# Kernel tuning notes

Hardware: AMD Instinct MI355X
Metric: run time of the kernel (lower is better)

## Reference

```python
import jax, jax.numpy as jnp
from jax import lax
import numpy as np

B, C, H, W = 4, 256, 64, 64
SPLIT = 8           # split_size
HEADS_BR = 4        # num_heads // 2 per branch
C2 = C // 2         # per-branch channels
HID = 4 * C         # mlp hidden
EPS = 1e-5


def layernorm(x, w, b):
    m = jnp.mean(x, -1, keepdims=True)
    v = jnp.mean((x - m) ** 2, -1, keepdims=True)
    return (x - m) * lax.rsqrt(v + EPS) * w + b


def lepe_attn(qk, v, gw, gb, Hsp, Wsp):
    # qk, v: (B, L, Cb) with L = H*W; windows of (Hsp, Wsp)
    Bq, L, Cb = qk.shape
    heads, hd = HEADS_BR, Cb // HEADS_BR
    nH, nW = H // Hsp, W // Wsp
    scale = hd ** -0.5
    # tokens -> windows -> heads: (B*nH*nW, heads, Hsp*Wsp, hd)
    qkw = (qk.reshape(Bq, nH, Hsp, nW, Wsp, Cb)
             .transpose(0, 1, 3, 2, 4, 5)
             .reshape(-1, Hsp * Wsp, heads, hd)
             .transpose(0, 2, 1, 3))
    # v as window images (B*nH*nW, Cb, Hsp, Wsp) for depthwise LePE conv
    vimg = (v.reshape(Bq, nH, Hsp, nW, Wsp, Cb)
              .transpose(0, 1, 3, 5, 2, 4)
              .reshape(-1, Cb, Hsp, Wsp))
    lepe = lax.conv_general_dilated(
        vimg, gw, (1, 1), 'SAME',
        dimension_numbers=('NCHW', 'OIHW', 'NCHW'),
        feature_group_count=Cb) + gb[None, :, None, None]
    vwin = vimg.reshape(-1, heads, hd, Hsp * Wsp).transpose(0, 1, 3, 2)
    lep = lepe.reshape(-1, heads, hd, Hsp * Wsp).transpose(0, 1, 3, 2)
    attn = jax.nn.softmax(
        jnp.einsum('whqd,whkd->whqk', qkw * scale, qkw), axis=-1)
    out = jnp.einsum('whqk,whkd->whqd', attn, vwin) + lep
    # windows -> image -> tokens
    out = (out.transpose(0, 2, 1, 3)
              .reshape(Bq, nH, nW, Hsp, Wsp, Cb)
              .transpose(0, 1, 3, 2, 4, 5)
              .reshape(Bq, L, Cb))
    return out


def setup_inputs() -> dict:
    key = jax.random.key(0)
    ks = jax.random.split(key, 8)
    p = lambda k, s: jax.random.normal(k, s, jnp.float32) * 0.02
    return {
        'x': jax.random.normal(ks[0], (B, C, H, W), jnp.float32),
        'norm1_w': jnp.ones((C,), jnp.float32),
        'norm1_b': jnp.zeros((C,), jnp.float32),
        'qkv_w': p(ks[1], (2 * C, C)),
        'getv_w0': p(ks[2], (C2, 1, 3, 3)),
        'getv_b0': jnp.zeros((C2,), jnp.float32),
        'getv_w1': p(ks[3], (C2, 1, 3, 3)),
        'getv_b1': jnp.zeros((C2,), jnp.float32),
        'proj_w': p(ks[4], (C, C)),
        'proj_b': jnp.zeros((C,), jnp.float32),
        'norm2_w': jnp.ones((C,), jnp.float32),
        'norm2_b': jnp.zeros((C,), jnp.float32),
        'fc1_w': p(ks[5], (HID, C)),
        'fc1_b': jnp.zeros((HID,), jnp.float32),
        'fc2_w': p(ks[6], (C, HID)),
        'fc2_b': jnp.zeros((C,), jnp.float32),
    }


def reference(x, norm1_w, norm1_b, qkv_w, getv_w0, getv_b0, getv_w1, getv_b1,
              proj_w, proj_b, norm2_w, norm2_b, fc1_w, fc1_b, fc2_w, fc2_b):
    b, c, h, w = x.shape
    x = x.reshape(b, c, h * w).transpose(0, 2, 1)        # (B, L, C)
    img = layernorm(x, norm1_w, norm1_b)
    qkv = img @ qkv_w.T                                  # (B, L, 2C)
    qk, v = qkv[..., :c], qkv[..., c:]                   # shared q=k, and v
    # branch 0: windows (H, split); branch 1: windows (split, W)
    x1 = lepe_attn(qk[..., :C2], v[..., :C2], getv_w0, getv_b0, h, SPLIT)
    x2 = lepe_attn(qk[..., C2:], v[..., C2:], getv_w1, getv_b1, SPLIT, w)
    att = jnp.concatenate([x1, x2], axis=2) @ proj_w.T + proj_b
    x = x + att
    y = layernorm(x, norm2_w, norm2_b)
    y = jax.nn.gelu(y @ fc1_w.T + fc1_b, approximate=False) @ fc2_w.T + fc2_b
    return x + y                                          # (B, L, C)
```

## Files before the change

kernel.cpp:

```cpp
#include <hip/hip_runtime.h>
#include <hip/hip_bf16.h>

#define BDIM 4
#define CDIM 256
#define HDIM 64
#define WDIM 64
#define LDIM 4096
#define ROWS 16384

typedef __attribute__((ext_vector_type(8))) short short8;
typedef __attribute__((ext_vector_type(4))) float f32x4;
typedef __attribute__((ext_vector_type(16))) float f32x16;
typedef unsigned int u32;

static __device__ __forceinline__ unsigned short f2bf(float f) {
    unsigned int x = __float_as_uint(f);
    unsigned int r = (x + 0x7fffu + ((x >> 16) & 1u)) >> 16;
    return (unsigned short)r;
}
static __device__ __forceinline__ float bf2f(unsigned int u) {
    return __uint_as_float(u << 16);
}
static __device__ __forceinline__ u32 pk2(float a, float b) {
    return (u32)f2bf(a) | ((u32)f2bf(b) << 16);
}

__global__ __launch_bounds__(256) void cvt4_kernel(
    const float* __restrict__ a, const float* __restrict__ b,
    const float* __restrict__ c, const float* __restrict__ d,
    unsigned short* __restrict__ oa, unsigned short* __restrict__ ob,
    unsigned short* __restrict__ oc, unsigned short* __restrict__ od)
{
    int i = blockIdx.x * 256 + threadIdx.x;
    const float* in; unsigned short* out; int off;
    if (i < 32768)       { in = a; out = oa; off = i; }
    else if (i < 49152)  { in = b; out = ob; off = i - 32768; }
    else if (i < 114688) { in = c; out = oc; off = i - 49152; }
    else if (i < 180224) { in = d; out = od; off = i - 114688; }
    else return;
    float4 f = reinterpret_cast<const float4*>(in)[off];
    reinterpret_cast<uint2*>(out)[off] = make_uint2(pk2(f.x, f.y), pk2(f.z, f.w));
}

__global__ __launch_bounds__(256) void norm_kernel(
    const float* __restrict__ xin,
    const float* __restrict__ w, const float* __restrict__ b,
    unsigned short* __restrict__ out,
    float* __restrict__ xT,
    int transposed_in)
{
    int wave = threadIdx.x >> 6;
    int lane = threadIdx.x & 63;
    int row = blockIdx.x * 4 + wave;
    float v[4];
    float sum = 0.f, sumsq = 0.f;
    if (transposed_in) {
        int bb = row >> 12;
        int l = row & 4095;
        const float* xb = xin + (size_t)bb * (CDIM * LDIM) + l;
        #pragma unroll
        for (int i = 0; i < 4; ++i) {
            int c = lane + i * 64;
            float t = xb[(size_t)c * LDIM];
            v[i] = t; sum += t; sumsq += t * t;
        }
    } else {
        const float* xr = xin + (size_t)row * CDIM;
        #pragma unroll
        for (int i = 0; i < 4; ++i) {
            float t = xr[lane + i * 64];
            v[i] = t; sum += t; sumsq += t * t;
        }
    }
    #pragma unroll
    for (int off = 32; off > 0; off >>= 1) {
        sum   += __shfl_xor(sum, off);
        sumsq += __shfl_xor(sumsq, off);
    }
    float mean = sum * (1.f / 256.f);
    float var  = sumsq * (1.f / 256.f) - mean * mean;
    float inv  = rsqrtf(var + 1e-5f);
    unsigned short* orow = out + (size_t)row * CDIM;
    #pragma unroll
    for (int i = 0; i < 4; ++i) {
        int c = lane + i * 64;
        if (xT) xT[(size_t)row * CDIM + c] = v[i];
        orow[c] = f2bf((v[i] - mean) * inv * w[c] + b[c]);
    }
}

__global__ __launch_bounds__(256) void mfma_gemm(
    const unsigned short* __restrict__ A,
    const unsigned short* __restrict__ Bm,
    const float* __restrict__ bias,
    const float* __restrict__ resid,
    void* __restrict__ outp,
    int N, int K, int mode)
{
    __shared__ unsigned short As[2][64 * 32];
    __shared__ unsigned short Bs[2][64 * 32];
    int tid  = threadIdx.x;
    int lane = tid & 63;
    int w    = tid >> 6;
    int wr   = w >> 1, wc = w & 1;
    int l15  = lane & 15, kbl = lane >> 4;

    int gx  = gridDim.x;
    int nwg = gx * gridDim.y;
    int bid = blockIdx.y * gx + blockIdx.x;
    int cpx = nwg >> 3;
    int swz = (bid & 7) * cpx + (bid >> 3);
    int n0 = (swz % gx) * 64;
    int m0 = (swz / gx) * 64;

    f32x4 acc[2][2];
    #pragma unroll
    for (int m = 0; m < 2; ++m)
        #pragma unroll
        for (int n = 0; n < 2; ++n)
            acc[m][n] = (f32x4){0.f, 0.f, 0.f, 0.f};

    int srow = tid >> 2;
    int sp   = tid & 3;
    int ss   = sp ^ (srow & 3);
    auto STAGE = [&](int buf, int k0) {
        const unsigned short* ga = A  + (size_t)(m0 + srow) * K + k0 + ss * 8;
        const unsigned short* gb = Bm + (size_t)(n0 + srow) * K + k0 + ss * 8;
        __builtin_amdgcn_global_load_lds(
            (const __attribute__((address_space(1))) void*)ga,
            (__attribute__((address_space(3))) void*)(As[buf] + tid * 8), 16, 0, 0);
        __builtin_amdgcn_global_load_lds(
            (const __attribute__((address_space(1))) void*)gb,
            (__attribute__((address_space(3))) void*)(Bs[buf] + tid * 8), 16, 0, 0);
    };

    STAGE(0, 0);
    __syncthreads();

    int cur = 0;
    for (int k0 = 0; k0 < K; k0 += 32) {
        if (k0 + 32 < K) STAGE(cur ^ 1, k0 + 32);

        short8 af[2], bf[2];
        #pragma unroll
        for (int m = 0; m < 2; ++m) {
            int row = wr * 32 + m * 16 + l15;
            af[m] = *reinterpret_cast<const short8*>(
                As[cur] + row * 32 + (kbl ^ (row & 3)) * 8);
        }
        #pragma unroll
        for (int n = 0; n < 2; ++n) {
            int row = wc * 32 + n * 16 + l15;
            bf[n] = *reinterpret_cast<const short8*>(
                Bs[cur] + row * 32 + (kbl ^ (row & 3)) * 8);
        }
        #pragma unroll
        for (int m = 0; m < 2; ++m)
            #pragma unroll
            for (int n = 0; n < 2; ++n)
                acc[m][n] = __builtin_amdgcn_mfma_f32_16x16x32_bf16(
                    af[m], bf[n], acc[m][n], 0, 0, 0);

        __syncthreads();
        cur ^= 1;
    }

    int r0 = kbl * 4;
    #pragma unroll
    for (int m = 0; m < 2; ++m) {
        #pragma unroll
        for (int n = 0; n < 2; ++n) {
            int col = n0 + wc * 32 + n * 16 + l15;
            #pragma unroll
            for (int r = 0; r < 4; ++r) {
                int row = m0 + wr * 32 + m * 16 + r0 + r;
                float v = acc[m][n][r];
                if (mode == 0) {
                    ((float*)outp)[(size_t)row * N + col] = v;
                } else if (mode == 1) {
                    ((unsigned short*)outp)[(size_t)row * N + col] = f2bf(v);
                } else if (mode == 2) {
                    v += bias[col];
                    v = 0.5f * v * (1.f + erff(v * 0.70710678118654752f));
                    ((unsigned short*)outp)[(size_t)row * N + col] = f2bf(v);
                } else {
                    v += bias[col] + resid[(size_t)row * N + col];
                    ((float*)outp)[(size_t)row * N + col] = v;
                }
            }
        }
    }
}

__global__ __launch_bounds__(512) void attn_kernel(
    const unsigned short* __restrict__ qkv,
    const float* __restrict__ gw0, const float* __restrict__ gb0,
    const float* __restrict__ gw1, const float* __restrict__ gb1,
    unsigned short* __restrict__ att)
{
    __shared__ unsigned short Kbuf[512 * 32];
    __shared__ unsigned short Vt[32 * 512];
    __shared__ float gwl[288];
    __shared__ float gbl[32];
    const int wh = blockIdx.x;
    const int br = wh >> 7, head = wh & 3, win = (wh >> 2) & 31;
    const int bb = win >> 3, wi = win & 7;
    const int tid = threadIdx.x;
    const int qk_off = br * 128 + head * 32;
    const int v_off = 256 + qk_off;
    const float sscale = 0.42044820762685725f;

    {
        const float* gw = br ? gw1 : gw0;
        const float* gb = br ? gb1 : gb0;
        if (tid < 288) gwl[tid] = gw[(head * 32) * 9 + tid];
        else if (tid >= 480) gbl[tid - 480] = gb[head * 32 + tid - 480];
    }
    {
        int t = tid;
        int l = (br == 0) ? ((t >> 3) * 64 + wi * 8 + (t & 7)) : (wi * 512 + t);
        const unsigned short* src = qkv + ((size_t)(bb * 4096 + l)) * 512 + qk_off;
        #pragma unroll
        for (int s = 0; s < 4; ++s) {
            uint4 raw = *reinterpret_cast<const uint4*>(src + s * 8);
            u32 rw[4] = {raw.x, raw.y, raw.z, raw.w};
            u32 ow[4];
            #pragma unroll
            for (int i = 0; i < 4; ++i) {
                float lo = bf2f(rw[i] & 0xffffu) * sscale;
                float hi = bf2f(rw[i] >> 16) * sscale;
                ow[i] = pk2(lo, hi);
            }
            int sl = s ^ ((t >> 1) & 3);
            *reinterpret_cast<uint4*>(Kbuf + t * 32 + sl * 8) =
                make_uint4(ow[0], ow[1], ow[2], ow[3]);
        }
    }
    {
        int kp = (tid & 255) * 2, dh = tid >> 8;
        int kq = kp + 1;
        int l0 = (br == 0) ? ((kp >> 3) * 64 + wi * 8 + (kp & 7)) : (wi * 512 + kp);
        int l1 = (br == 0) ? ((kq >> 3) * 64 + wi * 8 + (kq & 7)) : (wi * 512 + kq);
        const unsigned short* v0 = qkv + ((size_t)(bb * 4096 + l0)) * 512 + v_off + dh * 16;
        const unsigned short* v1 = qkv + ((size_t)(bb * 4096 + l1)) * 512 + v_off + dh * 16;
        uint4 a0 = *reinterpret_cast<const uint4*>(v0);
        uint4 a1 = *reinterpret_cast<const uint4*>(v0 + 8);
        uint4 b0 = *reinterpret_cast<const uint4*>(v1);
        uint4 b1 = *reinterpret_cast<const uint4*>(v1 + 8);
        u32 av[8] = {a0.x, a0.y, a0.z, a0.w, a1.x, a1.y, a1.z, a1.w};
        u32 bv[8] = {b0.x, b0.y, b0.z, b0.w, b1.x, b1.y, b1.z, b1.w};
        int slot = kp >> 3;
        #pragma unroll
        for (int dd = 0; dd < 16; ++dd) {
            u32 x0 = (dd & 1) ? (av[dd >> 1] >> 16) : (av[dd >> 1] & 0xffffu);
            u32 x1 = (dd & 1) ? (bv[dd >> 1] >> 16) : (bv[dd >> 1] & 0xffffu);
            int d = dh * 16 + dd;
            int sl = slot ^ (d & 7);
            *reinterpret_cast<u32*>(Vt + d * 512 + sl * 8 + (kp & 7)) = x0 | (x1 << 16);
        }
    }
    __syncthreads();

    const int lane = tid & 63;
    const int w = tid >> 6;
    const int ql = lane & 31;
    const int h = lane >> 5;
    const int q0 = w * 64;

    f32x16 O0, O1;
    #pragma unroll
    for (int i = 0; i < 16; ++i) { O0[i] = 0.f; O1[i] = 0.f; }
    float m0 = -1e30f, m1 = -1e30f, su0 = 0.f, su1 = 0.f;

    auto process = [&](int QS, f32x16& O, float& M, float& SU,
                       short8 kf0, short8 kf1, short8 vf0, short8 vf1) {
        int qrow = q0 + QS * 32 + ql;
        int sw = (qrow >> 1) & 3;
        short8 qf0 = *reinterpret_cast<const short8*>(Kbuf + qrow * 32 + ((0 + h) ^ sw) * 8);
        short8 qf1 = *reinterpret_cast<const short8*>(Kbuf + qrow * 32 + ((2 + h) ^ sw) * 8);
        f32x16 sacc;
        #pragma unroll
        for (int i = 0; i < 16; ++i) sacc[i] = 0.f;
        sacc = __builtin_amdgcn_mfma_f32_32x32x16_bf16(kf0, qf0, sacc, 0, 0, 0);
        sacc = __builtin_amdgcn_mfma_f32_32x32x16_bf16(kf1, qf1, sacc, 0, 0, 0);
        float mx = sacc[0];
        #pragma unroll
        for (int r = 1; r < 16; ++r) mx = fmaxf(mx, sacc[r]);
        mx = fmaxf(mx, __shfl_xor(mx, 32));
        float nm = fmaxf(M, mx);
        float fs = __expf(M - nm);
        M = nm;
        float p[16];
        float ps = 0.f;
        #pragma unroll
        for (int r = 0; r < 16; ++r) { p[r] = __expf(sacc[r] - nm); ps += p[r]; }
        ps += __shfl_xor(ps, 32);
        SU = SU * fs + ps;
        u32 P[8];
        #pragma unroll
        for (int g = 0; g < 4; ++g) {
            P[2 * g]     = pk2(p[4 * g],     p[4 * g + 1]);
            P[2 * g + 1] = pk2(p[4 * g + 2], p[4 * g + 3]);
        }
        u32 X[8];
        #pragma unroll
        for (int i = 0; i < 8; ++i) X[i] = __shfl_xor(P[i], 32);
        union { u32 u[4]; short8 s; } c0, c1;
        c0.u[0] = h ? X[2] : P[0];  c0.u[1] = h ? X[3] : P[1];
        c0.u[2] = h ? P[2] : X[0];  c0.u[3] = h ? P[3] : X[1];
        c1.u[0] = h ? X[6] : P[4];  c1.u[1] = h ? X[7] : P[5];
        c1.u[2] = h ? P[6] : X[4];  c1.u[3] = h ? P[7] : X[5];
        #pragma unroll
        for (int r = 0; r < 16; ++r) O[r] *= fs;
        O = __builtin_amdgcn_mfma_f32_32x32x16_bf16(vf0, c0.s, O, 0, 0, 0);
        O = __builtin_amdgcn_mfma_f32_32x32x16_bf16(vf1, c1.s, O, 0, 0, 0);
    };

    for (int kt = 0; kt < 16; ++kt) {
        int k0 = kt * 32;
        int krow = k0 + ql;
        int ksw = (krow >> 1) & 3;
        short8 kf0 = *reinterpret_cast<const short8*>(Kbuf + krow * 32 + ((0 + h) ^ ksw) * 8);
        short8 kf1 = *reinterpret_cast<const short8*>(Kbuf + krow * 32 + ((2 + h) ^ ksw) * 8);
        int ko0 = k0 + h * 8;
        int ko1 = k0 + 16 + h * 8;
        short8 vf0 = *reinterpret_cast<const short8*>(Vt + ql * 512 + ((ko0 >> 3) ^ (ql & 7)) * 8);
        short8 vf1 = *reinterpret_cast<const short8*>(Vt + ql * 512 + ((ko1 >> 3) ^ (ql & 7)) * 8);
        process(0, O0, m0, su0, kf0, kf1, vf0, vf1);
        process(1, O1, m1, su1, kf0, kf1, vf0, vf1);
    }

    #pragma unroll
    for (int QS = 0; QS < 2; ++QS) {
        f32x16& O = QS ? O1 : O0;
        float inv = 1.f / (QS ? su1 : su0);
        int qrow = q0 + QS * 32 + ql;
        int hs  = (br == 0) ? (qrow >> 3) : (qrow >> 6);
        int wsx = (br == 0) ? (qrow & 7)  : (qrow & 63);

        float lep[16];
        #pragma unroll
        for (int r = 0; r < 16; ++r) {
            int d = (r & 3) + 8 * (r >> 2) + 4 * h;
            lep[r] = gbl[d];
        }
        #pragma unroll
        for (int dy = -1; dy <= 1; ++dy) {
            int hn = hs + dy;
            bool okh = (br == 0) ? ((unsigned)hn < 64u) : ((unsigned)hn < 8u);
            #pragma unroll
            for (int dx = -1; dx <= 1; ++dx) {
                int wn = wsx + dx;
                bool okw = (br == 0) ? ((unsigned)wn < 8u) : ((unsigned)wn < 64u);
                if (okh && okw) {
                    int key = (br == 0) ? (hn * 8 + wn) : (hn * 64 + wn);
                    int t = (dy + 1) * 3 + (dx + 1);
                    #pragma unroll
                    for (int r = 0; r < 16; ++r) {
                        int d = (r & 3) + 8 * (r >> 2) + 4 * h;
                        float vv = bf2f((u32)(unsigned short)
                            Vt[d * 512 + (((key >> 3) ^ (d & 7)) * 8 + (key & 7))]);
                        lep[r] += vv * gwl[d * 9 + t];
                    }
                }
            }
        }

        int l = (br == 0) ? ((qrow >> 3) * 64 + wi * 8 + (qrow & 7)) : (wi * 512 + qrow);
        unsigned short* orow = att + ((size_t)(bb * 4096 + l)) * 256 + qk_off;
        #pragma unroll
        for (int g = 0; g < 4; ++g) {
            u32 lo = pk2(O[4 * g] * inv + lep[4 * g],
                         O[4 * g + 1] * inv + lep[4 * g + 1]);
            u32 hi = pk2(O[4 * g + 2] * inv + lep[4 * g + 2],
                         O[4 * g + 3] * inv + lep[4 * g + 3]);
            *reinterpret_cast<uint2*>(orow + 8 * g + 4 * h) = make_uint2(lo, hi);
        }
    }
}

extern "C" void kernel_launch(void* const* d_in, const int* in_sizes, int n_in,
                              void* d_out, int out_size, void* d_ws, size_t ws_size,
                              hipStream_t stream) {
    const float* x     = (const float*)d_in[0];
    const float* n1w   = (const float*)d_in[1];
    const float* n1b   = (const float*)d_in[2];
    const float* qkvw  = (const float*)d_in[3];
    const float* gw0   = (const float*)d_in[4];
    const float* gb0   = (const float*)d_in[5];
    const float* gw1   = (const float*)d_in[6];
    const float* gb1   = (const float*)d_in[7];
    const float* projw = (const float*)d_in[8];
    const float* projb = (const float*)d_in[9];
    const float* n2w   = (const float*)d_in[10];
    const float* n2b   = (const float*)d_in[11];
    const float* fc1w  = (const float*)d_in[12];
    const float* fc1b  = (const float*)d_in[13];
    const float* fc2w  = (const float*)d_in[14];
    const float* fc2b  = (const float*)d_in[15];
    float* out = (float*)d_out;
    char* wsb  = (char*)d_ws;

    float*          xT   = (float*)wsb;
    unsigned short* qkv  = (unsigned short*)(wsb + 16777216);
    unsigned short* att  = (unsigned short*)(wsb + 33554432);
    unsigned short* img  = (unsigned short*)(wsb + 41943040);
    unsigned short* wq   = (unsigned short*)(wsb + 50331648);
    unsigned short* wp   = (unsigned short*)(wsb + 50593792);
    unsigned short* w1   = (unsigned short*)(wsb + 50724864);
    unsigned short* w2   = (unsigned short*)(wsb + 51249152);
    unsigned short* ynorm  = img;
    unsigned short* hidden = (unsigned short*)wsb;

    cvt4_kernel<<<704, 256, 0, stream>>>(qkvw, projw, fc1w, fc2w, wq, wp, w1, w2);

    norm_kernel<<<4096, 256, 0, stream>>>(x, n1w, n1b, img, xT, 1);
    mfma_gemm<<<dim3(8, 256), 256, 0, stream>>>(img, wq, nullptr, nullptr, qkv, 512, 256, 1);
    attn_kernel<<<256, 512, 0, stream>>>(qkv, gw0, gb0, gw1, gb1, att);
    mfma_gemm<<<dim3(4, 256), 256, 0, stream>>>(att, wp, projb, xT, out, 256, 256, 3);
    norm_kernel<<<4096, 256, 0, stream>>>(out, n2w, n2b, ynorm, nullptr, 0);
    mfma_gemm<<<dim3(16, 256), 256, 0, stream>>>(ynorm, w1, fc1b, nullptr, hidden, 1024, 256, 2);
    mfma_gemm<<<dim3(4, 256), 256, 0, stream>>>(hidden, w2, fc2b, out, out, 256, 1024, 3);
}
```

Measured before the change: 162.4 us.

## Fuse weight conversion with first layernorm, widen GEMM K-tile, use tanh GELU

```diff
diff --git a/kernel.cpp b/kernel.cpp
--- a/kernel.cpp
+++ b/kernel.cpp
@@ -25,52 +25,74 @@
     return (u32)f2bf(a) | ((u32)f2bf(b) << 16);
 }
 
-__global__ __launch_bounds__(256) void cvt4_kernel(
-    const float* __restrict__ a, const float* __restrict__ b,
-    const float* __restrict__ c, const float* __restrict__ d,
-    unsigned short* __restrict__ oa, unsigned short* __restrict__ ob,
-    unsigned short* __restrict__ oc, unsigned short* __restrict__ od)
+__global__ __launch_bounds__(256) void prep_kernel(
+    const float* __restrict__ x,
+    const float* __restrict__ n1w, const float* __restrict__ n1b,
+    unsigned short* __restrict__ img, float* __restrict__ xT,
+    const float* __restrict__ qkvw, const float* __restrict__ projw,
+    const float* __restrict__ fc1w, const float* __restrict__ fc2w,
+    unsigned short* __restrict__ wq, unsigned short* __restrict__ wp,
+    unsigned short* __restrict__ w1, unsigned short* __restrict__ w2)
 {
-    int i = blockIdx.x * 256 + threadIdx.x;
-    const float* in; unsigned short* out; int off;
-    if (i < 32768)       { in = a; out = oa; off = i; }
-    else if (i < 49152)  { in = b; out = ob; off = i - 32768; }
-    else if (i < 114688) { in = c; out = oc; off = i - 49152; }
-    else if (i < 180224) { in = d; out = od; off = i - 114688; }
-    else return;
-    float4 f = reinterpret_cast<const float4*>(in)[off];
-    reinterpret_cast<uint2*>(out)[off] = make_uint2(pk2(f.x, f.y), pk2(f.z, f.w));
+    int blk = blockIdx.x;
+    if (blk < 704) {
+        int i = blk * 256 + threadIdx.x;
+        const float* in; unsigned short* out; int off;
+        if (i < 32768)       { in = qkvw; out = wq; off = i; }
+        else if (i < 49152)  { in = projw; out = wp; off = i - 32768; }
+        else if (i < 114688) { in = fc1w; out = w1; off = i - 49152; }
+        else if (i < 180224) { in = fc2w; out = w2; off = i - 114688; }
+        else return;
+        float4 f = reinterpret_cast<const float4*>(in)[off];
+        reinterpret_cast<uint2*>(out)[off] = make_uint2(pk2(f.x, f.y), pk2(f.z, f.w));
+        return;
+    }
+    int wave = threadIdx.x >> 6;
+    int lane = threadIdx.x & 63;
+    int row = (blk - 704) * 4 + wave;
+    int bb = row >> 12;
+    int l = row & 4095;
+    const float* xb = x + (size_t)bb * (CDIM * LDIM) + l;
+    float v[4];
+    float sum = 0.f, sumsq = 0.f;
+    #pragma unroll
+    for (int i = 0; i < 4; ++i) {
+        int c = lane + i * 64;
+        float t = xb[(size_t)c * LDIM];
+        v[i] = t; sum += t; sumsq += t * t;
+    }
+    #pragma unroll
+    for (int off = 32; off > 0; off >>= 1) {
+        sum   += __shfl_xor(sum, off);
+        sumsq += __shfl_xor(sumsq, off);
+    }
+    float mean = sum * (1.f / 256.f);
+    float var  = sumsq * (1.f / 256.f) - mean * mean;
+    float inv  = rsqrtf(var + 1e-5f);
+    unsigned short* orow = img + (size_t)row * CDIM;
+    #pragma unroll
+    for (int i = 0; i < 4; ++i) {
+        int c = lane + i * 64;
+        xT[(size_t)row * CDIM + c] = v[i];
+        orow[c] = f2bf((v[i] - mean) * inv * n1w[c] + n1b[c]);
+    }
 }
 
 __global__ __launch_bounds__(256) void norm_kernel(
     const float* __restrict__ xin,
     const float* __restrict__ w, const float* __restrict__ b,
-    unsigned short* __restrict__ out,
-    float* __restrict__ xT,
-    int transposed_in)
+    unsigned short* __restrict__ out)
 {
     int wave = threadIdx.x >> 6;
     int lane = threadIdx.x & 63;
     int row = blockIdx.x * 4 + wave;
+    const float* xr = xin + (size_t)row * CDIM;
     float v[4];
     float sum = 0.f, sumsq = 0.f;
-    if (transposed_in) {
-        int bb = row >> 12;
-        int l = row & 4095;
-        const float* xb = xin + (size_t)bb * (CDIM * LDIM) + l;
-        #pragma unroll
-        for (int i = 0; i < 4; ++i) {
-            int c = lane + i * 64;
-            float t = xb[(size_t)c * LDIM];
-            v[i] = t; sum += t; sumsq += t * t;
-        }
-    } else {
-        const float* xr = xin + (size_t)row * CDIM;
-        #pragma unroll
-        for (int i = 0; i < 4; ++i) {
-            float t = xr[lane + i * 64];
-            v[i] = t; sum += t; sumsq += t * t;
-        }
+    #pragma unroll
+    for (int i = 0; i < 4; ++i) {
+        float t = xr[lane + i * 64];
+        v[i] = t; sum += t; sumsq += t * t;
     }
     #pragma unroll
     for (int off = 32; off > 0; off >>= 1) {
@@ -84,7 +106,6 @@
     #pragma unroll
     for (int i = 0; i < 4; ++i) {
         int c = lane + i * 64;
-        if (xT) xT[(size_t)row * CDIM + c] = v[i];
         orow[c] = f2bf((v[i] - mean) * inv * w[c] + b[c]);
     }
 }
@@ -97,8 +118,8 @@
     void* __restrict__ outp,
     int N, int K, int mode)
 {
-    __shared__ unsigned short As[2][64 * 32];
-    __shared__ unsigned short Bs[2][64 * 32];
+    __shared__ unsigned short As[2][64 * 64];
+    __shared__ unsigned short Bs[2][64 * 64];
     int tid  = threadIdx.x;
     int lane = tid & 63;
     int w    = tid >> 6;
@@ -120,46 +141,53 @@
         for (int n = 0; n < 2; ++n)
             acc[m][n] = (f32x4){0.f, 0.f, 0.f, 0.f};
 
-    int srow = tid >> 2;
-    int sp   = tid & 3;
-    int ss   = sp ^ (srow & 3);
     auto STAGE = [&](int buf, int k0) {
-        const unsigned short* ga = A  + (size_t)(m0 + srow) * K + k0 + ss * 8;
-        const unsigned short* gb = Bm + (size_t)(n0 + srow) * K + k0 + ss * 8;
-        __builtin_amdgcn_global_load_lds(
-            (const __attribute__((address_space(1))) void*)ga,
-            (__attribute__((address_space(3))) void*)(As[buf] + tid * 8), 16, 0, 0);
-        __builtin_amdgcn_global_load_lds(
-            (const __attribute__((address_space(1))) void*)gb,
-            (__attribute__((address_space(3))) void*)(Bs[buf] + tid * 8), 16, 0, 0);
+        #pragma unroll
+        for (int i = 0; i < 2; ++i) {
+            int c = i * 256 + tid;
+            int row = c >> 3, p = c & 7;
+            int g = p ^ (row & 7);
+            const unsigned short* ga = A  + (size_t)(m0 + row) * K + k0 + g * 8;
+            const unsigned short* gb = Bm + (size_t)(n0 + row) * K + k0 + g * 8;
+            __builtin_amdgcn_global_load_lds(
+                (const __attribute__((address_space(1))) void*)ga,
+                (__attribute__((address_space(3))) void*)(As[buf] + c * 8), 16, 0, 0);
+            __builtin_amdgcn_global_load_lds(
+                (const __attribute__((address_space(1))) void*)gb,
+                (__attribute__((address_space(3))) void*)(Bs[buf] + c * 8), 16, 0, 0);
+        }
     };
 
     STAGE(0, 0);
     __syncthreads();
 
     int cur = 0;
-    for (int k0 = 0; k0 < K; k0 += 32) {
-        if (k0 + 32 < K) STAGE(cur ^ 1, k0 + 32);
-
-        short8 af[2], bf[2];
-        #pragma unroll
-        for (int m = 0; m < 2; ++m) {
-            int row = wr * 32 + m * 16 + l15;
-            af[m] = *reinterpret_cast<const short8*>(
-                As[cur] + row * 32 + (kbl ^ (row & 3)) * 8);
-        }
-        #pragma unroll
-        for (int n = 0; n < 2; ++n) {
-            int row = wc * 32 + n * 16 + l15;
-            bf[n] = *reinterpret_cast<const short8*>(
-                Bs[cur] + row * 32 + (kbl ^ (row & 3)) * 8);
-        }
-        #pragma unroll
-        for (int m = 0; m < 2; ++m)
-            #pragma unroll
-            for (int n = 0; n < 2; ++n)
-                acc[m][n] = __builtin_amdgcn_mfma_f32_16x16x32_bf16(
-                    af[m], bf[n], acc[m][n], 0, 0, 0);
+    for (int k0 = 0; k0 < K; k0 += 64) {
+        if (k0 + 64 < K) STAGE(cur ^ 1, k0 + 64);
+
+        #pragma unroll
+        for (int ks = 0; ks < 2; ++ks) {
+            int kg = ks * 4 + kbl;
+            short8 af[2], bf[2];
+            #pragma unroll
+            for (int m = 0; m < 2; ++m) {
+                int row = wr * 32 + m * 16 + l15;
+                af[m] = *reinterpret_cast<const short8*>(
+                    As[cur] + row * 64 + (kg ^ (row & 7)) * 8);
+            }
+            #pragma unroll
+            for (int n = 0; n < 2; ++n) {
+                int row = wc * 32 + n * 16 + l15;
+                bf[n] = *reinterpret_cast<const short8*>(
+                    Bs[cur] + row * 64 + (kg ^ (row & 7)) * 8);
+            }
+            #pragma unroll
+            for (int m = 0; m < 2; ++m)
+                #pragma unroll
+                for (int n = 0; n < 2; ++n)
+                    acc[m][n] = __builtin_amdgcn_mfma_f32_16x16x32_bf16(
+                        af[m], bf[n], acc[m][n], 0, 0, 0);
+        }
 
         __syncthreads();
         cur ^= 1;
@@ -181,7 +209,11 @@
                     ((unsigned short*)outp)[(size_t)row * N + col] = f2bf(v);
                 } else if (mode == 2) {
                     v += bias[col];
-                    v = 0.5f * v * (1.f + erff(v * 0.70710678118654752f));
+                    float u = v * (0.7978845608f + 0.0356774081f * v * v);
+                    float t = exp2f(-2.8853900818f * fabsf(u));
+                    float th = __fdividef(1.f - t, 1.f + t);
+                    th = copysignf(th, u);
+                    v = 0.5f * v * (1.f + th);
                     ((unsigned short*)outp)[(size_t)row * N + col] = f2bf(v);
                 } else {
                     v += bias[col] + resid[(size_t)row * N + col];
@@ -412,13 +444,12 @@
     unsigned short* ynorm  = img;
     unsigned short* hidden = (unsigned short*)wsb;
 
-    cvt4_kernel<<<704, 256, 0, stream>>>(qkvw, projw, fc1w, fc2w, wq, wp, w1, w2);
-
-    norm_kernel<<<4096, 256, 0, stream>>>(x, n1w, n1b, img, xT, 1);
+    prep_kernel<<<4800, 256, 0, stream>>>(x, n1w, n1b, img, xT,
+                                          qkvw, projw, fc1w, fc2w, wq, wp, w1, w2);
     mfma_gemm<<<dim3(8, 256), 256, 0, stream>>>(img, wq, nullptr, nullptr, qkv, 512, 256, 1);
     attn_kernel<<<256, 512, 0, stream>>>(qkv, gw0, gb0, gw1, gb1, att);
     mfma_gemm<<<dim3(4, 256), 256, 0, stream>>>(att, wp, projb, xT, out, 256, 256, 3);
-    norm_kernel<<<4096, 256, 0, stream>>>(out, n2w, n2b, ynorm, nullptr, 0);
+    norm_kernel<<<4096, 256, 0, stream>>>(out, n2w, n2b, ynorm);
     mfma_gemm<<<dim3(16, 256), 256, 0, stream>>>(ynorm, w1, fc1b, nullptr, hidden, 1024, 256, 2);
     mfma_gemm<<<dim3(4, 256), 256, 0, stream>>>(hidden, w2, fc2b, out, out, 256, 1024, 3);
 }
```

Result: no change. 159.3 us (-1.9%).
